# Optimization experiments

Hardware: AMD Instinct MI355X
Metric: run time of the kernel (lower is better)

Reference implementation:

```python
import jax, jax.numpy as jnp
import numpy as np

N_NODES = 50000
N_EDGES = 800000
IN_C, HID_C, OUT_C = 512, 256, 2


def gcn_conv(x, W, b, src, dst, norm, num_nodes):
    # x: [N, Fin]; W: [Fin, Fout]; src/dst/norm: [E+N] (self-loops included)
    h = x @ W                                   # [N, Fout]
    msgs = h[src] * norm[:, None]               # gather + scale, [E+N, Fout]
    out = jax.ops.segment_sum(msgs, dst, num_segments=num_nodes)  # scatter-add
    return out + b


def _gcn_norm(src, dst, num_nodes):
    # PyG gcn_norm with add_self_loops=True, unit edge weights
    loop = jnp.arange(num_nodes, dtype=src.dtype)
    src2 = jnp.concatenate([src, loop])
    dst2 = jnp.concatenate([dst, loop])
    w = jnp.ones(src2.shape[0], dtype=jnp.float32)
    deg = jax.ops.segment_sum(w, dst2, num_segments=num_nodes)
    dinv = jnp.where(deg > 0, jax.lax.rsqrt(deg), 0.0)
    norm = dinv[src2] * dinv[dst2]
    return src2, dst2, norm


def setup_inputs() -> dict:
    key = jax.random.key(0)
    ks = jax.random.split(key, 4)
    x = jax.random.normal(ks[0], (N_NODES, IN_C), dtype=jnp.float32)
    edge_index = jax.random.randint(ks[1], (2, N_EDGES), 0, N_NODES, dtype=jnp.int64)
    W1 = jax.random.normal(ks[2], (IN_C, HID_C), dtype=jnp.float32) / np.sqrt(IN_C)
    b1 = jnp.zeros((HID_C,), dtype=jnp.float32)
    W2 = jax.random.normal(ks[3], (HID_C, OUT_C), dtype=jnp.float32) / np.sqrt(HID_C)
    b2 = jnp.zeros((OUT_C,), dtype=jnp.float32)
    return {"x": x, "edge_index": edge_index, "W1": W1, "b1": b1, "W2": W2, "b2": b2}


def reference(x, edge_index, W1, b1, W2, b2):
    n = x.shape[0]
    src, dst, norm = _gcn_norm(edge_index[0], edge_index[1], n)
    h = gcn_conv(x, W1, b1, src, dst, norm, n)
    h = jax.nn.relu(h)
    # dropout is identity in eval mode (training=False)
    out = gcn_conv(h, W2, b2, src, dst, norm, n)
    return out
```

## Files before the change

kernel.cpp:

```cpp
#include <hip/hip_runtime.h>
#include <hip/hip_bf16.h>
#include <stdint.h>

#define N_NODES 50000
#define N_EDGES 800000
#define IN_C 512
#define HID_C 256
#define CAP 96

typedef __attribute__((ext_vector_type(8))) short bf16x8;
typedef __attribute__((ext_vector_type(4))) float f32x4;
typedef __attribute__((address_space(3))) uint32_t lds_u32_t;
typedef __attribute__((address_space(1))) const uint32_t g_u32_t;

__device__ __forceinline__ void g2l16(const void* g, void* l) {
    __builtin_amdgcn_global_load_lds((g_u32_t*)g, (lds_u32_t*)l, 16, 0, 0);
}

__device__ __forceinline__ unsigned short f2bf(float f) {
    uint32_t u = __float_as_uint(f);
    uint32_t r = (u + 0x7fff + ((u >> 16) & 1)) >> 16;
    return (unsigned short)r;
}


#define ZERO_BLOCKS ((N_NODES + 255) / 256)
#define PREP_BLOCKS (ZERO_BLOCKS + 256)

__global__ __launch_bounds__(256) void prep_kernel(int* __restrict__ cursor,
                                                   const float* __restrict__ W1,
                                                   unsigned short* __restrict__ Wt) {
    const int t = threadIdx.x;
    if (blockIdx.x < ZERO_BLOCKS) {
        const int i = blockIdx.x * 256 + t;
        if (i < N_NODES) cursor[i] = 0;
    } else {
        const int c = blockIdx.x - ZERO_BLOCKS;
        for (int k = t; k < IN_C; k += 256)
            Wt[c * IN_C + k] = f2bf(W1[k * HID_C + c]);
    }
}


#define GEMM_BLOCKS ((N_NODES + 127) / 128)
#define FILL_BLOCKS ((N_EDGES + 1023) / 1024)
#define GF_BLOCKS (GEMM_BLOCKS + FILL_BLOCKS)
#define NKT 16

__global__ __launch_bounds__(512) void gf_kernel(
    const float* __restrict__ A,
    const unsigned short* __restrict__ Bt,
    unsigned short* __restrict__ hB,
    int M,
    const int* __restrict__ src,
    const int* __restrict__ dst,
    int* cursor,
    unsigned short* __restrict__ bucket)
{
    __shared__ float          Asf[2][128 * 32];
    __shared__ unsigned short Bs[2][256 * 32];
    const int t = threadIdx.x;

    if (blockIdx.x >= GEMM_BLOCKS) {
        const int i0 = ((blockIdx.x - GEMM_BLOCKS) * 512 + t) * 2;
        if (i0 >= N_EDGES) return;
        int s0, d0, s1 = -1, d1 = -1;
        if (i0 + 2 <= N_EDGES) {
            const int2 s2 = *(const int2*)&src[i0];
            const int2 d2 = *(const int2*)&dst[i0];
            s0 = s2.x; s1 = s2.y; d0 = d2.x; d1 = d2.y;
        } else {
            s0 = src[i0]; d0 = dst[i0];
        }
        const int p0 = atomicAdd(&cursor[d0], 1);
        if (p0 < CAP) bucket[d0 * CAP + p0] = (unsigned short)s0;
        if (s1 >= 0) {
            const int p1 = atomicAdd(&cursor[d1], 1);
            if (p1 < CAP) bucket[d1 * CAP + p1] = (unsigned short)s1;
        }
        return;
    }

    const int m0 = blockIdx.x * 128;
    const int w = t >> 6, l = t & 63;
    const int wr = (w >> 2) * 64;
    const int wc = (w & 3) * 64;
    const int l15 = l & 15, l4 = l >> 4;

    f32x4 acc[4][4] = {};

    auto stage = [&](int buf, int kt) {
        #pragma unroll
        for (int q = 0; q < 2; ++q) {
            const int idx = q * 512 + t;
            const int row = idx >> 3;
            const int ck  = (idx & 7) ^ (row & 7);
            int gr = m0 + row; if (gr >= M) gr = M - 1;
            g2l16(&A[(size_t)gr * IN_C + kt * 32 + ck * 4], &Asf[buf][idx * 4]);
        }
        #pragma unroll
        for (int q = 0; q < 2; ++q) {
            const int idx = q * 512 + t;
            const int row = idx >> 2;
            const int ck  = (idx & 3) ^ (row & 3) ^ ((row >> 2) & 3);
            g2l16(&Bt[(size_t)row * IN_C + kt * 32 + ck * 8], &Bs[buf][idx * 8]);
        }
    };
    auto compute = [&](int buf) {
        bf16x8 a[4], b[4];
        #pragma unroll
        for (int mi = 0; mi < 4; ++mi) {
            const int r  = wr + mi * 16 + l15;
            const int s0 = l4 * 2;
            const float4 lo = *(const float4*)&Asf[buf][r * 32 + ((s0    ) ^ (r & 7)) * 4];
            const float4 hi = *(const float4*)&Asf[buf][r * 32 + ((s0 + 1) ^ (r & 7)) * 4];
            union { bf16x8 v; __hip_bfloat162 h2[4]; } cv;
            cv.h2[0] = __float22bfloat162_rn(make_float2(lo.x, lo.y));
            cv.h2[1] = __float22bfloat162_rn(make_float2(lo.z, lo.w));
            cv.h2[2] = __float22bfloat162_rn(make_float2(hi.x, hi.y));
            cv.h2[3] = __float22bfloat162_rn(make_float2(hi.z, hi.w));
            a[mi] = cv.v;
        }
        #pragma unroll
        for (int nj = 0; nj < 4; ++nj) {
            const int r  = wc + nj * 16 + l15;
            const int ck = l4 ^ (r & 3) ^ ((r >> 2) & 3);
            b[nj] = *(const bf16x8*)&Bs[buf][r * 32 + ck * 8];
        }
        #pragma unroll
        for (int mi = 0; mi < 4; ++mi)
            #pragma unroll
            for (int nj = 0; nj < 4; ++nj)
                acc[mi][nj] = __builtin_amdgcn_mfma_f32_16x16x32_bf16(
                    a[mi], b[nj], acc[mi][nj], 0, 0, 0);
    };

    stage(0, 0);
    asm volatile("s_waitcnt vmcnt(0)" ::: "memory");
    __builtin_amdgcn_s_barrier();
    int cur = 0;
    for (int kt = 0; kt < NKT; ++kt) {
        if (kt < NKT - 1) {
            stage(cur ^ 1, kt + 1);
            asm volatile("s_waitcnt vmcnt(4)" ::: "memory");
        } else {
            asm volatile("s_waitcnt vmcnt(0)" ::: "memory");
        }
        __builtin_amdgcn_s_barrier();
        compute(cur);
        __builtin_amdgcn_s_barrier();
        cur ^= 1;
    }

    #pragma unroll
    for (int mi = 0; mi < 4; ++mi)
        #pragma unroll
        for (int nj = 0; nj < 4; ++nj)
            #pragma unroll
            for (int rr = 0; rr < 4; ++rr) {
                const int m = m0 + wr + mi * 16 + l4 * 4 + rr;
                const int n = wc + nj * 16 + l15;
                if (m < M) hB[(size_t)m * HID_C + n] = f2bf(acc[mi][nj][rr]);
            }
}


__global__ void dinv_kernel(const int* __restrict__ cursor,
                            float* __restrict__ dinv, int n) {
    const int i = blockIdx.x * 256 + threadIdx.x;
    if (i < n) dinv[i] = rsqrtf((float)(cursor[i] + 1));
}


__device__ __forceinline__ void fma8(float* acc, uint4 r, float w) {
    acc[0] += __uint_as_float((r.x & 0xffffu) << 16) * w;
    acc[1] += __uint_as_float(r.x & 0xffff0000u) * w;
    acc[2] += __uint_as_float((r.y & 0xffffu) << 16) * w;
    acc[3] += __uint_as_float(r.y & 0xffff0000u) * w;
    acc[4] += __uint_as_float((r.z & 0xffffu) << 16) * w;
    acc[5] += __uint_as_float(r.z & 0xffff0000u) * w;
    acc[6] += __uint_as_float((r.w & 0xffffu) << 16) * w;
    acc[7] += __uint_as_float(r.w & 0xffff0000u) * w;
}

__global__ __launch_bounds__(256) void agg1_kernel(const unsigned short* __restrict__ h,
                                                   const int* __restrict__ cursor,
                                                   const unsigned short* __restrict__ bucket,
                                                   const float* __restrict__ dinv,
                                                   const float* __restrict__ b1,
                                                   const float* __restrict__ W2,
                                                   float* __restrict__ h2) {
    const int node = blockIdx.x * 8 + (threadIdx.x >> 5);
    const int g = threadIdx.x & 31;
    const int f0 = g << 3;
    int cnt = cursor[node]; if (cnt > CAP) cnt = CAP;
    const float dv_d = dinv[node];

    float acc[8] = {};
    {
        const uint4 rs = *(const uint4*)&h[(size_t)node * HID_C + f0];
        fma8(acc, rs, dv_d);
    }

    const unsigned short* bkt = &bucket[node * CAP];
    for (int base = 0; base < cnt; base += 32) {
        const int rem = cnt - base;
        const int c32 = rem < 32 ? rem : 32;
        int idx = 0; float dv_s = 0.f;
        if (g < c32) {
            idx  = bkt[base + g];
            dv_s = dinv[idx];
        }
        int i = 0;
        for (; i + 4 <= c32; i += 4) {
            const int   i0 = __shfl(idx, i,     32); const float w0 = __shfl(dv_s, i,     32);
            const int   i1 = __shfl(idx, i + 1, 32); const float w1 = __shfl(dv_s, i + 1, 32);
            const int   i2 = __shfl(idx, i + 2, 32); const float w2 = __shfl(dv_s, i + 2, 32);
            const int   i3 = __shfl(idx, i + 3, 32); const float w3 = __shfl(dv_s, i + 3, 32);
            const uint4 r0 = *(const uint4*)&h[(size_t)i0 * HID_C + f0];
            const uint4 r1 = *(const uint4*)&h[(size_t)i1 * HID_C + f0];
            const uint4 r2 = *(const uint4*)&h[(size_t)i2 * HID_C + f0];
            const uint4 r3 = *(const uint4*)&h[(size_t)i3 * HID_C + f0];
            fma8(acc, r0, w0); fma8(acc, r1, w1); fma8(acc, r2, w2); fma8(acc, r3, w3);
        }
        for (; i < c32; ++i) {
            const int   ii = __shfl(idx, i, 32);
            const float w  = __shfl(dv_s, i, 32);
            const uint4 r  = *(const uint4*)&h[(size_t)ii * HID_C + f0];
            fma8(acc, r, w);
        }
    }

    const float4 ba = *(const float4*)&b1[f0];
    const float4 bb = *(const float4*)&b1[f0 + 4];
    float v[8];
    v[0] = fmaxf(acc[0] * dv_d + ba.x, 0.f); v[1] = fmaxf(acc[1] * dv_d + ba.y, 0.f);
    v[2] = fmaxf(acc[2] * dv_d + ba.z, 0.f); v[3] = fmaxf(acc[3] * dv_d + ba.w, 0.f);
    v[4] = fmaxf(acc[4] * dv_d + bb.x, 0.f); v[5] = fmaxf(acc[5] * dv_d + bb.y, 0.f);
    v[6] = fmaxf(acc[6] * dv_d + bb.z, 0.f); v[7] = fmaxf(acc[7] * dv_d + bb.w, 0.f);

    float c0 = 0.f, c1 = 0.f;
    #pragma unroll
    for (int q = 0; q < 4; ++q) {
        const float4 wv = *(const float4*)&W2[f0 * 2 + q * 4];
        c0 += v[2*q] * wv.x + v[2*q+1] * wv.z;
        c1 += v[2*q] * wv.y + v[2*q+1] * wv.w;
    }
    #pragma unroll
    for (int o = 16; o > 0; o >>= 1) {
        c0 += __shfl_down(c0, o, 32);
        c1 += __shfl_down(c1, o, 32);
    }
    if (g == 0) *(float2*)&h2[node * 2] = make_float2(c0, c1);
}


__global__ void agg2_kernel(const float* __restrict__ h2,
                            const int* __restrict__ cursor,
                            const unsigned short* __restrict__ bucket,
                            const float* __restrict__ dinv,
                            const float* __restrict__ b2,
                            float* __restrict__ out, int n_nodes) {
    const int n = blockIdx.x * blockDim.x + threadIdx.x;
    if (n >= n_nodes) return;
    int cnt = cursor[n]; if (cnt > CAP) cnt = CAP;
    const float dv_d = dinv[n];
    const float2 ps = *(const float2*)&h2[n * 2];
    float a0 = dv_d * ps.x, a1 = dv_d * ps.y;
    const unsigned short* bkt = &bucket[n * CAP];
    int i = 0;
    for (; i + 4 <= cnt; i += 4) {
        const uint2 q4 = *(const uint2*)&bkt[i];
        const int s0 = q4.x & 0xffff, s1 = q4.x >> 16;
        const int s2 = q4.y & 0xffff, s3 = q4.y >> 16;
        const float w0 = dinv[s0], w1 = dinv[s1];
        const float w2 = dinv[s2], w3 = dinv[s3];
        const float2 p0 = *(const float2*)&h2[s0 * 2];
        const float2 p1 = *(const float2*)&h2[s1 * 2];
        const float2 p2 = *(const float2*)&h2[s2 * 2];
        const float2 p3 = *(const float2*)&h2[s3 * 2];
        a0 += p0.x * w0 + p1.x * w1 + p2.x * w2 + p3.x * w3;
        a1 += p0.y * w0 + p1.y * w1 + p2.y * w2 + p3.y * w3;
    }
    for (; i < cnt; ++i) {
        const int s = bkt[i];
        const float w = dinv[s];
        const float2 p = *(const float2*)&h2[s * 2];
        a0 += p.x * w;
        a1 += p.y * w;
    }
    out[n * 2 + 0] = b2[0] + dv_d * a0;
    out[n * 2 + 1] = b2[1] + dv_d * a1;
}


static inline size_t align_up(size_t x) { return (x + 255) & ~(size_t)255; }

extern "C" void kernel_launch(void* const* d_in, const int* in_sizes, int n_in,
                              void* d_out, int out_size, void* d_ws, size_t ws_size,
                              hipStream_t stream) {
    const float* x   = (const float*)d_in[0];
    const int*   ei  = (const int*)d_in[1];
    const float* W1  = (const float*)d_in[2];
    const float* b1  = (const float*)d_in[3];
    const float* W2  = (const float*)d_in[4];
    const float* b2  = (const float*)d_in[5];
    float* out = (float*)d_out;

    const int* e_src = ei;
    const int* e_dst = ei + N_EDGES;

    char* ws = (char*)d_ws;
    int*   cursor   = (int*)ws;             ws += align_up((size_t)N_NODES * 4);
    float* dinv     = (float*)ws;           ws += align_up((size_t)N_NODES * 4);
    unsigned short* bucket = (unsigned short*)ws; ws += align_up((size_t)N_NODES * CAP * 2);
    unsigned short* Wt = (unsigned short*)ws; ws += align_up((size_t)HID_C * IN_C * 2);
    unsigned short* h  = (unsigned short*)ws; ws += align_up((size_t)N_NODES * HID_C * 2);
    float* h2       = (float*)ws;           ws += align_up((size_t)N_NODES * 2 * 4);

    const int nb_n = (N_NODES + 255) / 256;

    prep_kernel<<<PREP_BLOCKS, 256, 0, stream>>>(cursor, W1, Wt);
    gf_kernel<<<GF_BLOCKS, 512, 0, stream>>>(x, Wt, h, N_NODES,
                                             e_src, e_dst, cursor, bucket);
    dinv_kernel<<<nb_n, 256, 0, stream>>>(cursor, dinv, N_NODES);
    agg1_kernel<<<N_NODES / 8, 256, 0, stream>>>(h, cursor, bucket, dinv, b1, W2, h2);
    agg2_kernel<<<nb_n, 256, 0, stream>>>(h2, cursor, bucket, dinv, b2, out, N_NODES);
}
```

Before: 129.5 us.

## Halve GEMM tile height and fold dinv computation into aggregation kernels

The GEMM part of the fused gemm/fill kernel now uses 64-row tiles instead of 128, which doubles the block count and cuts LDS per block. That should give more blocks for occupancy and tail balance, at the cost of fewer MFMAs per B-tile load. The separate dinv kernel and its buffer are removed. Both aggregation kernels now compute rsqrt(degree+1) directly from the cursor array, saving a launch and a pass over memory in exchange for extra rsqrt work in the gather loops.

```diff
diff --git a/kernel.cpp b/kernel.cpp
--- a/kernel.cpp
+++ b/kernel.cpp
@@ -42,7 +42,7 @@
 }
 
 
-#define GEMM_BLOCKS ((N_NODES + 127) / 128)
+#define GEMM_BLOCKS ((N_NODES + 63) / 64)
 #define FILL_BLOCKS ((N_EDGES + 1023) / 1024)
 #define GF_BLOCKS (GEMM_BLOCKS + FILL_BLOCKS)
 #define NKT 16
@@ -57,7 +57,7 @@
     int* cursor,
     unsigned short* __restrict__ bucket)
 {
-    __shared__ float          Asf[2][128 * 32];
+    __shared__ float          Asf[2][64 * 32];
     __shared__ unsigned short Bs[2][256 * 32];
     const int t = threadIdx.x;
 
@@ -81,18 +81,17 @@
         return;
     }
 
-    const int m0 = blockIdx.x * 128;
+    const int m0 = blockIdx.x * 64;
     const int w = t >> 6, l = t & 63;
-    const int wr = (w >> 2) * 64;
+    const int wr = (w >> 2) * 32;
     const int wc = (w & 3) * 64;
     const int l15 = l & 15, l4 = l >> 4;
 
-    f32x4 acc[4][4] = {};
+    f32x4 acc[2][4] = {};
 
     auto stage = [&](int buf, int kt) {
-        #pragma unroll
-        for (int q = 0; q < 2; ++q) {
-            const int idx = q * 512 + t;
+        {
+            const int idx = t;
             const int row = idx >> 3;
             const int ck  = (idx & 7) ^ (row & 7);
             int gr = m0 + row; if (gr >= M) gr = M - 1;
@@ -107,9 +106,9 @@
         }
     };
     auto compute = [&](int buf) {
-        bf16x8 a[4], b[4];
-        #pragma unroll
-        for (int mi = 0; mi < 4; ++mi) {
+        bf16x8 a[2], b[4];
+        #pragma unroll
+        for (int mi = 0; mi < 2; ++mi) {
             const int r  = wr + mi * 16 + l15;
             const int s0 = l4 * 2;
             const float4 lo = *(const float4*)&Asf[buf][r * 32 + ((s0    ) ^ (r & 7)) * 4];
@@ -128,7 +127,7 @@
             b[nj] = *(const bf16x8*)&Bs[buf][r * 32 + ck * 8];
         }
         #pragma unroll
-        for (int mi = 0; mi < 4; ++mi)
+        for (int mi = 0; mi < 2; ++mi)
             #pragma unroll
             for (int nj = 0; nj < 4; ++nj)
                 acc[mi][nj] = __builtin_amdgcn_mfma_f32_16x16x32_bf16(
@@ -142,7 +141,7 @@
     for (int kt = 0; kt < NKT; ++kt) {
         if (kt < NKT - 1) {
             stage(cur ^ 1, kt + 1);
-            asm volatile("s_waitcnt vmcnt(4)" ::: "memory");
+            asm volatile("s_waitcnt vmcnt(3)" ::: "memory");
         } else {
             asm volatile("s_waitcnt vmcnt(0)" ::: "memory");
         }
@@ -153,7 +152,7 @@
     }
 
     #pragma unroll
-    for (int mi = 0; mi < 4; ++mi)
+    for (int mi = 0; mi < 2; ++mi)
         #pragma unroll
         for (int nj = 0; nj < 4; ++nj)
             #pragma unroll
@@ -162,13 +161,6 @@
                 const int n = wc + nj * 16 + l15;
                 if (m < M) hB[(size_t)m * HID_C + n] = f2bf(acc[mi][nj][rr]);
             }
-}
-
-
-__global__ void dinv_kernel(const int* __restrict__ cursor,
-                            float* __restrict__ dinv, int n) {
-    const int i = blockIdx.x * 256 + threadIdx.x;
-    if (i < n) dinv[i] = rsqrtf((float)(cursor[i] + 1));
 }
 
 
@@ -183,10 +175,13 @@
     acc[7] += __uint_as_float(r.w & 0xffff0000u) * w;
 }
 
+__device__ __forceinline__ float dinv_of(const int* cursor, int n) {
+    return rsqrtf((float)(cursor[n] + 1));
+}
+
 __global__ __launch_bounds__(256) void agg1_kernel(const unsigned short* __restrict__ h,
                                                    const int* __restrict__ cursor,
                                                    const unsigned short* __restrict__ bucket,
-                                                   const float* __restrict__ dinv,
                                                    const float* __restrict__ b1,
                                                    const float* __restrict__ W2,
                                                    float* __restrict__ h2) {
@@ -194,7 +189,7 @@
     const int g = threadIdx.x & 31;
     const int f0 = g << 3;
     int cnt = cursor[node]; if (cnt > CAP) cnt = CAP;
-    const float dv_d = dinv[node];
+    const float dv_d = rsqrtf((float)(cursor[node] + 1));
 
     float acc[8] = {};
     {
@@ -209,7 +204,7 @@
         int idx = 0; float dv_s = 0.f;
         if (g < c32) {
             idx  = bkt[base + g];
-            dv_s = dinv[idx];
+            dv_s = dinv_of(cursor, idx);
         }
         int i = 0;
         for (; i + 4 <= c32; i += 4) {
@@ -258,13 +253,12 @@
 __global__ void agg2_kernel(const float* __restrict__ h2,
                             const int* __restrict__ cursor,
                             const unsigned short* __restrict__ bucket,
-                            const float* __restrict__ dinv,
                             const float* __restrict__ b2,
                             float* __restrict__ out, int n_nodes) {
     const int n = blockIdx.x * blockDim.x + threadIdx.x;
     if (n >= n_nodes) return;
     int cnt = cursor[n]; if (cnt > CAP) cnt = CAP;
-    const float dv_d = dinv[n];
+    const float dv_d = rsqrtf((float)(cursor[n] + 1));
     const float2 ps = *(const float2*)&h2[n * 2];
     float a0 = dv_d * ps.x, a1 = dv_d * ps.y;
     const unsigned short* bkt = &bucket[n * CAP];
@@ -273,8 +267,10 @@
         const uint2 q4 = *(const uint2*)&bkt[i];
         const int s0 = q4.x & 0xffff, s1 = q4.x >> 16;
         const int s2 = q4.y & 0xffff, s3 = q4.y >> 16;
-        const float w0 = dinv[s0], w1 = dinv[s1];
-        const float w2 = dinv[s2], w3 = dinv[s3];
+        const float w0 = rsqrtf((float)(cursor[s0] + 1));
+        const float w1 = rsqrtf((float)(cursor[s1] + 1));
+        const float w2 = rsqrtf((float)(cursor[s2] + 1));
+        const float w3 = rsqrtf((float)(cursor[s3] + 1));
         const float2 p0 = *(const float2*)&h2[s0 * 2];
         const float2 p1 = *(const float2*)&h2[s1 * 2];
         const float2 p2 = *(const float2*)&h2[s2 * 2];
@@ -284,7 +280,7 @@
     }
     for (; i < cnt; ++i) {
         const int s = bkt[i];
-        const float w = dinv[s];
+        const float w = rsqrtf((float)(cursor[s] + 1));
         const float2 p = *(const float2*)&h2[s * 2];
         a0 += p.x * w;
         a1 += p.y * w;
@@ -312,7 +308,6 @@
 
     char* ws = (char*)d_ws;
     int*   cursor   = (int*)ws;             ws += align_up((size_t)N_NODES * 4);
-    float* dinv     = (float*)ws;           ws += align_up((size_t)N_NODES * 4);
     unsigned short* bucket = (unsigned short*)ws; ws += align_up((size_t)N_NODES * CAP * 2);
     unsigned short* Wt = (unsigned short*)ws; ws += align_up((size_t)HID_C * IN_C * 2);
     unsigned short* h  = (unsigned short*)ws; ws += align_up((size_t)N_NODES * HID_C * 2);
@@ -323,7 +318,6 @@
     prep_kernel<<<PREP_BLOCKS, 256, 0, stream>>>(cursor, W1, Wt);
     gf_kernel<<<GF_BLOCKS, 512, 0, stream>>>(x, Wt, h, N_NODES,
                                              e_src, e_dst, cursor, bucket);
-    dinv_kernel<<<nb_n, 256, 0, stream>>>(cursor, dinv, N_NODES);
-    agg1_kernel<<<N_NODES / 8, 256, 0, stream>>>(h, cursor, bucket, dinv, b1, W2, h2);
-    agg2_kernel<<<nb_n, 256, 0, stream>>>(h2, cursor, bucket, dinv, b2, out, N_NODES);
-}
+    agg1_kernel<<<N_NODES / 8, 256, 0, stream>>>(h, cursor, bucket, b1, W2, h2);
+    agg2_kernel<<<nb_n, 256, 0, stream>>>(h2, cursor, bucket, b2, out, N_NODES);
+}
```

Measured after the change: 168.0 us. 1.3x slower.

## Replicate per-node edge bucket cursors to spread atomic contention

Applied to the files above, without the earlier changes.

Splits each node's adjacency bucket and counter into eight replicas selected by fill-block index, so atomics on the same destination from different blocks hit different counters. The degree and aggregation kernels now sum the eight replica counts and walk the replica sub-buckets using prefix offsets. This targets atomic serialization and contention during the CSR-like fill. In exchange it costs a larger cursor array to zero, bigger bucket storage, extra index math per edge in agg1, and scattered sub-bucket reads.

```diff
diff --git a/kernel.cpp b/kernel.cpp
--- a/kernel.cpp
+++ b/kernel.cpp
@@ -6,7 +6,8 @@
 #define N_EDGES 800000
 #define IN_C 512
 #define HID_C 256
-#define CAP 96
+#define NREP 8
+#define CAP_R 32
 
 typedef __attribute__((ext_vector_type(8))) short bf16x8;
 typedef __attribute__((ext_vector_type(4))) float f32x4;
@@ -24,7 +25,7 @@
 }
 
 
-#define ZERO_BLOCKS ((N_NODES + 255) / 256)
+#define ZERO_BLOCKS ((N_NODES * NREP + 255) / 256)
 #define PREP_BLOCKS (ZERO_BLOCKS + 256)
 
 __global__ __launch_bounds__(256) void prep_kernel(int* __restrict__ cursor,
@@ -33,7 +34,7 @@
     const int t = threadIdx.x;
     if (blockIdx.x < ZERO_BLOCKS) {
         const int i = blockIdx.x * 256 + t;
-        if (i < N_NODES) cursor[i] = 0;
+        if (i < N_NODES * NREP) cursor[i] = 0;
     } else {
         const int c = blockIdx.x - ZERO_BLOCKS;
         for (int k = t; k < IN_C; k += 256)
@@ -62,7 +63,9 @@
     const int t = threadIdx.x;
 
     if (blockIdx.x >= GEMM_BLOCKS) {
-        const int i0 = ((blockIdx.x - GEMM_BLOCKS) * 512 + t) * 2;
+        const int fb = blockIdx.x - GEMM_BLOCKS;
+        const int rep = fb & (NREP - 1);
+        const int i0 = (fb * 512 + t) * 2;
         if (i0 >= N_EDGES) return;
         int s0, d0, s1 = -1, d1 = -1;
         if (i0 + 2 <= N_EDGES) {
@@ -72,11 +75,11 @@
         } else {
             s0 = src[i0]; d0 = dst[i0];
         }
-        const int p0 = atomicAdd(&cursor[d0], 1);
-        if (p0 < CAP) bucket[d0 * CAP + p0] = (unsigned short)s0;
+        const int p0 = atomicAdd(&cursor[d0 * NREP + rep], 1);
+        if (p0 < CAP_R) bucket[(d0 * NREP + rep) * CAP_R + p0] = (unsigned short)s0;
         if (s1 >= 0) {
-            const int p1 = atomicAdd(&cursor[d1], 1);
-            if (p1 < CAP) bucket[d1 * CAP + p1] = (unsigned short)s1;
+            const int p1 = atomicAdd(&cursor[d1 * NREP + rep], 1);
+            if (p1 < CAP_R) bucket[(d1 * NREP + rep) * CAP_R + p1] = (unsigned short)s1;
         }
         return;
     }
@@ -168,7 +171,11 @@
 __global__ void dinv_kernel(const int* __restrict__ cursor,
                             float* __restrict__ dinv, int n) {
     const int i = blockIdx.x * 256 + threadIdx.x;
-    if (i < n) dinv[i] = rsqrtf((float)(cursor[i] + 1));
+    if (i >= n) return;
+    const int4 ca = *(const int4*)&cursor[i * NREP];
+    const int4 cb = *(const int4*)&cursor[i * NREP + 4];
+    const int deg = 1 + ca.x + ca.y + ca.z + ca.w + cb.x + cb.y + cb.z + cb.w;
+    dinv[i] = rsqrtf((float)deg);
 }
 
 
@@ -193,8 +200,22 @@
     const int node = blockIdx.x * 8 + (threadIdx.x >> 5);
     const int g = threadIdx.x & 31;
     const int f0 = g << 3;
-    int cnt = cursor[node]; if (cnt > CAP) cnt = CAP;
+
+    const int4 ca = *(const int4*)&cursor[node * NREP];
+    const int4 cb = *(const int4*)&cursor[node * NREP + 4];
+    int off[9];
+    off[0] = 0;
+    off[1] = off[0] + min(ca.x, CAP_R);
+    off[2] = off[1] + min(ca.y, CAP_R);
+    off[3] = off[2] + min(ca.z, CAP_R);
+    off[4] = off[3] + min(ca.w, CAP_R);
+    off[5] = off[4] + min(cb.x, CAP_R);
+    off[6] = off[5] + min(cb.y, CAP_R);
+    off[7] = off[6] + min(cb.z, CAP_R);
+    off[8] = off[7] + min(cb.w, CAP_R);
+    const int total = off[8];
     const float dv_d = dinv[node];
+    const unsigned short* bkt = &bucket[(size_t)node * NREP * CAP_R];
 
     float acc[8] = {};
     {
@@ -202,13 +223,16 @@
         fma8(acc, rs, dv_d);
     }
 
-    const unsigned short* bkt = &bucket[node * CAP];
-    for (int base = 0; base < cnt; base += 32) {
-        const int rem = cnt - base;
+    for (int base = 0; base < total; base += 32) {
+        const int rem = total - base;
         const int c32 = rem < 32 ? rem : 32;
         int idx = 0; float dv_s = 0.f;
         if (g < c32) {
-            idx  = bkt[base + g];
+            const int e = base + g;
+            int r = 0;
+            #pragma unroll
+            for (int q = 1; q < 8; ++q) r += (e >= off[q]);
+            idx  = bkt[r * CAP_R + (e - off[r])];
             dv_s = dinv[idx];
         }
         int i = 0;
@@ -263,31 +287,35 @@
                             float* __restrict__ out, int n_nodes) {
     const int n = blockIdx.x * blockDim.x + threadIdx.x;
     if (n >= n_nodes) return;
-    int cnt = cursor[n]; if (cnt > CAP) cnt = CAP;
     const float dv_d = dinv[n];
     const float2 ps = *(const float2*)&h2[n * 2];
     float a0 = dv_d * ps.x, a1 = dv_d * ps.y;
-    const unsigned short* bkt = &bucket[n * CAP];
-    int i = 0;
-    for (; i + 4 <= cnt; i += 4) {
-        const uint2 q4 = *(const uint2*)&bkt[i];
-        const int s0 = q4.x & 0xffff, s1 = q4.x >> 16;
-        const int s2 = q4.y & 0xffff, s3 = q4.y >> 16;
-        const float w0 = dinv[s0], w1 = dinv[s1];
-        const float w2 = dinv[s2], w3 = dinv[s3];
-        const float2 p0 = *(const float2*)&h2[s0 * 2];
-        const float2 p1 = *(const float2*)&h2[s1 * 2];
-        const float2 p2 = *(const float2*)&h2[s2 * 2];
-        const float2 p3 = *(const float2*)&h2[s3 * 2];
-        a0 += p0.x * w0 + p1.x * w1 + p2.x * w2 + p3.x * w3;
-        a1 += p0.y * w0 + p1.y * w1 + p2.y * w2 + p3.y * w3;
-    }
-    for (; i < cnt; ++i) {
-        const int s = bkt[i];
-        const float w = dinv[s];
-        const float2 p = *(const float2*)&h2[s * 2];
-        a0 += p.x * w;
-        a1 += p.y * w;
+    const unsigned short* bkt = &bucket[(size_t)n * NREP * CAP_R];
+    #pragma unroll
+    for (int r = 0; r < NREP; ++r) {
+        int cr = cursor[n * NREP + r]; if (cr > CAP_R) cr = CAP_R;
+        const unsigned short* b = &bkt[r * CAP_R];
+        int i = 0;
+        for (; i + 4 <= cr; i += 4) {
+            const uint2 q4 = *(const uint2*)&b[i];
+            const int s0 = q4.x & 0xffff, s1 = q4.x >> 16;
+            const int s2 = q4.y & 0xffff, s3 = q4.y >> 16;
+            const float w0 = dinv[s0], w1 = dinv[s1];
+            const float w2 = dinv[s2], w3 = dinv[s3];
+            const float2 p0 = *(const float2*)&h2[s0 * 2];
+            const float2 p1 = *(const float2*)&h2[s1 * 2];
+            const float2 p2 = *(const float2*)&h2[s2 * 2];
+            const float2 p3 = *(const float2*)&h2[s3 * 2];
+            a0 += p0.x * w0 + p1.x * w1 + p2.x * w2 + p3.x * w3;
+            a1 += p0.y * w0 + p1.y * w1 + p2.y * w2 + p3.y * w3;
+        }
+        for (; i < cr; ++i) {
+            const int s = b[i];
+            const float w = dinv[s];
+            const float2 p = *(const float2*)&h2[s * 2];
+            a0 += p.x * w;
+            a1 += p.y * w;
+        }
     }
     out[n * 2 + 0] = b2[0] + dv_d * a0;
     out[n * 2 + 1] = b2[1] + dv_d * a1;
@@ -311,9 +339,9 @@
     const int* e_dst = ei + N_EDGES;
 
     char* ws = (char*)d_ws;
-    int*   cursor   = (int*)ws;             ws += align_up((size_t)N_NODES * 4);
+    int*   cursor   = (int*)ws;             ws += align_up((size_t)N_NODES * NREP * 4);
     float* dinv     = (float*)ws;           ws += align_up((size_t)N_NODES * 4);
-    unsigned short* bucket = (unsigned short*)ws; ws += align_up((size_t)N_NODES * CAP * 2);
+    unsigned short* bucket = (unsigned short*)ws; ws += align_up((size_t)N_NODES * NREP * CAP_R * 2);
     unsigned short* Wt = (unsigned short*)ws; ws += align_up((size_t)HID_C * IN_C * 2);
     unsigned short* h  = (unsigned short*)ws; ws += align_up((size_t)N_NODES * HID_C * 2);
     float* h2       = (float*)ws;           ws += align_up((size_t)N_NODES * 2 * 4);
```

After: 140.5 us. 8.5% more time.
